# Optimization experiments

Measured on AMD Instinct MI355X. Metric: run time of the kernel, lower is better.

The kernel has to match this reference:

```python
import jax, jax.numpy as jnp
import numpy as np

NUM_NODES = 100000
N = 65536          # subgraph nodes returned by LastNeighborLoader
E = 655360         # N * size(=10) last-neighbor edges
B = 4096           # temporal event batch
MEM = 128          # memory_dim (== pos_embedding_dim)
TIME = 64          # time_dim
MSG = 64           # raw_msg_dim
EMB = 128          # embedding_dim (gnn out_channels)
HEADS = 2
HD = EMB // HEADS  # 64, TransformerConv out_channels//2 per head
HID = 64           # mlp_hidden_dim[-1]
IN = 2 * MEM       # gnn in_channels (memory || pos memory)
EDGE_D = MSG + TIME


def setup_inputs() -> dict:
    key = jax.random.key(0)
    ks = jax.random.split(key, 32)
    nrm = lambda i, shp, s=1.0: jax.random.normal(ks[i], shp, jnp.float32) * s
    inp = {}
    # data / state tensors
    inp["memory"] = nrm(0, (NUM_NODES, MEM))
    inp["pos_memory"] = nrm(1, (NUM_NODES, MEM))
    inp["last_update"] = jax.random.uniform(ks[2], (NUM_NODES,), jnp.float32) * 1000.0
    inp["n_id"] = jnp.arange(N, dtype=jnp.int32)
    inp["edge_index"] = jax.random.randint(ks[3], (2, E), 0, N, dtype=jnp.int32)
    inp["edge_t"] = jax.random.uniform(ks[4], (E,), jnp.float32) * 1000.0
    inp["edge_msg"] = nrm(5, (E, MSG))
    inp["src"] = jax.random.randint(ks[6], (B,), 0, N, dtype=jnp.int32)
    inp["dst"] = jax.random.randint(ks[7], (B,), 0, N, dtype=jnp.int32)
    inp["neg_dst"] = jax.random.randint(ks[8], (B,), 0, N, dtype=jnp.int32)
    # learned parameters
    inp["time_w"] = nrm(9, (1, TIME))                      # TimeEncoder Linear(1, time_dim)
    inp["time_b"] = nrm(10, (TIME,), 0.1)
    sI = 1.0 / np.sqrt(IN); sE = 1.0 / np.sqrt(EDGE_D)
    inp["Wq"] = nrm(11, (IN, HEADS * HD), sI); inp["bq"] = jnp.zeros((HEADS * HD,), jnp.float32)
    inp["Wk"] = nrm(12, (IN, HEADS * HD), sI); inp["bk"] = jnp.zeros((HEADS * HD,), jnp.float32)
    inp["Wv"] = nrm(13, (IN, HEADS * HD), sI); inp["bv"] = jnp.zeros((HEADS * HD,), jnp.float32)
    inp["We"] = nrm(14, (EDGE_D, HEADS * HD), sE); inp["be"] = jnp.zeros((HEADS * HD,), jnp.float32)
    inp["Wskip"] = nrm(15, (IN, EMB), sI); inp["bskip"] = jnp.zeros((EMB,), jnp.float32)
    inp["mlp_w"] = nrm(16, (EMB, HID), 1.0 / np.sqrt(EMB)); inp["mlp_b"] = jnp.zeros((HID,), jnp.float32)
    sH = 1.0 / np.sqrt(HID)
    inp["lps_w"] = nrm(17, (HID, HID), sH); inp["lps_b"] = jnp.zeros((HID,), jnp.float32)
    inp["lpd_w"] = nrm(18, (HID, HID), sH); inp["lpd_b"] = jnp.zeros((HID,), jnp.float32)
    inp["lpf_w"] = nrm(19, (HID, 1), sH); inp["lpf_b"] = jnp.zeros((1,), jnp.float32)
    return inp


def reference(memory, pos_memory, last_update, n_id, edge_index, edge_t, edge_msg,
              src, dst, neg_dst, time_w, time_b, Wq, bq, Wk, bk, Wv, bv, We, be,
              Wskip, bskip, mlp_w, mlp_b, lps_w, lps_b, lpd_w, lpd_b, lpf_w, lpf_b):
    Nn = n_id.shape[0]
    # assoc remap: global node id -> local row in subgraph
    assoc = jnp.zeros((NUM_NODES,), jnp.int32).at[n_id].set(jnp.arange(Nn, dtype=jnp.int32))
    # memory read + positional memory concat  -> [N, 2*MEM]
    z = jnp.concatenate([memory[n_id], pos_memory[n_id]], axis=-1)
    lu = last_update[n_id]                                # [N]
    se, de = edge_index[0], edge_index[1]                 # source (j), target (i)
    # time encoding of relative time: cos(Linear(1->TIME))
    rel_t = lu[se] - edge_t                               # [E]
    t_enc = jnp.cos(rel_t[:, None] * time_w[0][None, :] + time_b)  # [E, TIME]
    edge_attr = jnp.concatenate([t_enc, edge_msg], axis=-1)        # [E, TIME+MSG]
    # TransformerConv (heads=2, concat): q from target, k/v from source (+edge)
    q = (z @ Wq + bq).reshape(Nn, HEADS, HD)
    k = (z @ Wk + bk).reshape(Nn, HEADS, HD)
    v = (z @ Wv + bv).reshape(Nn, HEADS, HD)
    e = (edge_attr @ We + be).reshape(-1, HEADS, HD)
    ke = k[se] + e                                        # [E, H, HD]
    ve = v[se] + e
    score = jnp.sum(q[de] * ke, axis=-1) / jnp.sqrt(jnp.float32(HD))  # [E, H]
    # segment softmax over incoming edges of each target node
    smax = jax.ops.segment_max(score, de, num_segments=Nn)
    ex = jnp.exp(score - smax[de])
    denom = jax.ops.segment_sum(ex, de, num_segments=Nn)
    alpha = ex / (denom[de] + 1e-16)                      # [E, H]
    agg = jax.ops.segment_sum(alpha[..., None] * ve, de, num_segments=Nn)  # [N, H, HD]
    out = agg.reshape(Nn, HEADS * HD) + (z @ Wskip + bskip)  # root/skip connection
    # MLP([embedding_dim, hidden]) -> single Linear (last layer: no act/norm)
    h = out @ mlp_w + mlp_b                               # [N, HID]
    z_src = h[assoc[src]]; z_dst = h[assoc[dst]]; z_neg = h[assoc[neg_dst]]
    def link_pred(a, b):
        hh = jax.nn.relu(a @ lps_w + lps_b + b @ lpd_w + lpd_b)
        return hh @ lpf_w + lpf_b
    pos_out = link_pred(z_src, z_dst)                     # [B, 1]
    neg_out = link_pred(z_src, z_neg)                     # [B, 1]
    return pos_out, neg_out
```

## Files before the change

kernel.cpp:

```cpp
#include <hip/hip_runtime.h>
#include <math.h>

#define NNODES 100000
#define NSUB   65536
#define NEDGE  655360
#define NBATCH 4096
#define LDK 72

typedef __attribute__((ext_vector_type(8))) short short8;
typedef __attribute__((ext_vector_type(4))) float f32x4;

__device__ __forceinline__ unsigned short f2bf(float x) {
  unsigned int b = __float_as_uint(x);
  b += 0x7fffu + ((b >> 16) & 1u);
  return (unsigned short)(b >> 16);
}
__device__ __forceinline__ float bf2f(unsigned short u) {
  return __uint_as_float(((unsigned int)u) << 16);
}
__device__ __forceinline__ unsigned int pk2(float a, float b) {
  return (unsigned int)f2bf(a) | ((unsigned int)f2bf(b) << 16);
}

__global__ void k_sentinel(float* out) { out[0] = -12345.0f; }

__global__ void k_packW(const float* __restrict__ Wq, const float* __restrict__ bq,
                        const float* __restrict__ Wk, const float* __restrict__ bk,
                        const float* __restrict__ Wv, const float* __restrict__ bv,
                        const float* __restrict__ Ws, const float* __restrict__ bs,
                        const float* __restrict__ We,
                        unsigned short* __restrict__ Wt, float* __restrict__ bias) {
  int n = blockIdx.x, r = threadIdx.x;
  float v = 0.f, bn = 0.f;
  if (n < 128) { v = Wq[r * 128 + n]; bn = bq[n]; }
  else if (n < 256) { int i = n - 128, l = i >> 1, h = i & 1; v = Wk[r * 128 + h * 64 + l]; bn = bk[h * 64 + l]; }
  else if (n < 384) { int i = n - 256, l = i >> 1, h = i & 1; v = Wv[r * 128 + h * 64 + l]; bn = bv[h * 64 + l]; }
  else if (n < 512) { int c = n - 384; v = Ws[r * 128 + c]; bn = bs[c]; }
  else {
    int i = n - 512, h = i >> 7, kk = i & 127;
    float s = 0.f;
    for (int c = 0; c < 64; c++) s += Wq[r * 128 + h * 64 + c] * We[kk * 128 + h * 64 + c];
    v = s;
    if (r == 0) { float sb = 0.f; for (int c = 0; c < 64; c++) sb += bq[h * 64 + c] * We[kk * 128 + h * 64 + c]; bn = sb; }
  }
  Wt[(size_t)n * 256 + r] = f2bf(v);
  if (r == 0) bias[n] = bn;
}

__global__ void k_packW2(const float* __restrict__ We, const float* __restrict__ mlp_w,
                         unsigned short* __restrict__ W2t) {
  int r = blockIdx.x, j = threadIdx.x;
  float v;
  if (r < 128) v = mlp_w[r * 64 + j];
  else if (r < 192) { int k = r - 128; float s = 0; for (int c = 0; c < 64; c++) s += We[k * 128 + c] * mlp_w[c * 64 + j]; v = s; }
  else if (r < 256) { int k = r - 192; float s = 0; for (int c = 0; c < 64; c++) s += We[(64 + k) * 128 + c] * mlp_w[c * 64 + j]; v = s; }
  else if (r < 320) { int k = r - 256; float s = 0; for (int c = 0; c < 64; c++) s += We[k * 128 + 64 + c] * mlp_w[(64 + c) * 64 + j]; v = s; }
  else if (r < 384) { int k = r - 320; float s = 0; for (int c = 0; c < 64; c++) s += We[(64 + k) * 128 + 64 + c] * mlp_w[(64 + c) * 64 + j]; v = s; }
  else v = mlp_w[(r - 384) * 64 + j];
  W2t[(size_t)j * 512 + r] = f2bf(v);
}

__global__ void k_bem(const float* __restrict__ be, const float* __restrict__ mlp_w,
                      float* __restrict__ bem) {
  int h = blockIdx.x, j = threadIdx.x;
  float s = 0.f;
  for (int c = 0; c < 64; c++) s += be[h * 64 + c] * mlp_w[(h * 64 + c) * 64 + j];
  bem[h * 64 + j] = s;
}

__global__ void k_assoc(const int* __restrict__ n_id, int* __restrict__ assoc) {
  int i = blockIdx.x * 256 + threadIdx.x;
  if (i < NSUB) assoc[n_id[i]] = i;
}

__global__ void k_relt(const int* __restrict__ edge_index, const int* __restrict__ n_id,
                       const float* __restrict__ last_update, const float* __restrict__ edge_t,
                       float* __restrict__ rel_t) {
  int e = blockIdx.x * 256 + threadIdx.x;
  if (e < NEDGE) rel_t[e] = last_update[n_id[edge_index[e]]] - edge_t[e];
}

__global__ void k_deg(const int* __restrict__ edge_index, int* __restrict__ deg) {
  int e = blockIdx.x * 256 + threadIdx.x;
  if (e < NEDGE) atomicAdd(&deg[edge_index[NEDGE + e]], 1);
}

__global__ __launch_bounds__(1024)
void k_scan(const int* __restrict__ deg, int* __restrict__ offs, int* __restrict__ cursor) {
  __shared__ int wsum[16];
  __shared__ int carry_s;
  int t = threadIdx.x, w = t >> 6, l = t & 63;
  if (t == 0) carry_s = 0;
  __syncthreads();
  for (int base = 0; base < NSUB; base += 1024) {
    int i = base + t;
    int v = deg[i];
    int s = v;
    #pragma unroll
    for (int d = 1; d < 64; d <<= 1) {
      int u = __shfl_up(s, d, 64);
      if (l >= d) s += u;
    }
    if (l == 63) wsum[w] = s;
    __syncthreads();
    int woff = 0;
    for (int k2 = 0; k2 < w; k2++) woff += wsum[k2];
    int total = 0;
    for (int k2 = 0; k2 < 16; k2++) total += wsum[k2];
    int c = carry_s;
    int excl = c + woff + s - v;
    offs[i] = excl; cursor[i] = excl;
    __syncthreads();
    if (t == 0) carry_s = c + total;
    __syncthreads();
  }
  if (t == 0) { offs[NSUB] = carry_s; cursor[NSUB] = carry_s; }
}

__global__ void k_scatter(const int* __restrict__ edge_index, int* __restrict__ cursor,
                          int* __restrict__ csr) {
  int e = blockIdx.x * 256 + threadIdx.x;
  if (e < NEDGE) {
    int p = atomicAdd(&cursor[edge_index[NEDGE + e]], 1);
    csr[p] = e;
  }
}

__global__ __launch_bounds__(256)
void k_gemm_node(const float* __restrict__ mem, const float* __restrict__ pmem,
                 const int* __restrict__ n_id, const unsigned short* __restrict__ Wt,
                 const float* __restrict__ bias, unsigned short* __restrict__ nodeout) {
  __shared__ unsigned short sA[128][LDK];
  __shared__ unsigned short sB[128][LDK];
  int t = threadIdx.x;
  int row0 = blockIdx.x * 128, n0 = blockIdx.y * 128;
  int ar = t >> 1, ak = (t & 1) * 32;
  int nid = n_id[row0 + ar];
  const float* arow0 = mem + (size_t)nid * 128;
  const float* arow1 = pmem + (size_t)nid * 128;
  int br = t >> 1;
  int w = t >> 6, lane = t & 63, quad = lane >> 4, r16 = lane & 15;
  int m_off = (w >> 1) * 64, n_off = (w & 1) * 64;
  f32x4 acc[4][4] = {};
  for (int st = 0; st < 4; st++) {
    int ks = st * 64;
    const float* src = (ks < 128) ? (arow0 + ks + ak) : (arow1 + (ks - 128) + ak);
    __syncthreads();
    #pragma unroll
    for (int i = 0; i < 8; i++) {
      float4 f = *(const float4*)(src + i * 4);
      *(uint2*)&sA[ar][ak + i * 4] = make_uint2(pk2(f.x, f.y), pk2(f.z, f.w));
    }
    #pragma unroll
    for (int j = 0; j < 4; j++) {
      int c = (t & 1) * 4 + j;
      *(uint4*)&sB[br][c * 8] = *(const uint4*)(Wt + (size_t)(n0 + br) * 256 + ks + c * 8);
    }
    __syncthreads();
    #pragma unroll
    for (int kk = 0; kk < 2; kk++) {
      short8 af[4], bf_[4];
      #pragma unroll
      for (int i = 0; i < 4; i++) af[i]  = *(const short8*)&sA[m_off + i * 16 + r16][kk * 32 + quad * 8];
      #pragma unroll
      for (int i = 0; i < 4; i++) bf_[i] = *(const short8*)&sB[n_off + i * 16 + r16][kk * 32 + quad * 8];
      #pragma unroll
      for (int i = 0; i < 4; i++)
        #pragma unroll
        for (int j = 0; j < 4; j++)
          acc[i][j] = __builtin_amdgcn_mfma_f32_16x16x32_bf16(af[i], bf_[j], acc[i][j], 0, 0, 0);
    }
  }
  #pragma unroll
  for (int j = 0; j < 4; j++) {
    int col = n0 + n_off + j * 16 + r16;
    float bv_ = bias[col];
    #pragma unroll
    for (int i = 0; i < 4; i++) {
      int rbase = row0 + m_off + i * 16 + quad * 4;
      #pragma unroll
      for (int rg = 0; rg < 4; rg++)
        nodeout[(size_t)(rbase + rg) * 768 + col] = f2bf(acc[i][j][rg] + bv_);
    }
  }
}

__global__ __launch_bounds__(256)
void k_edge(const unsigned short* __restrict__ nodeout, const int* __restrict__ edge_index,
            const float* __restrict__ rel_t, const float* __restrict__ edge_msg,
            const float* __restrict__ time_w, const float* __restrict__ time_b,
            const float* __restrict__ be, const int* __restrict__ offs,
            const int* __restrict__ csr, unsigned short* __restrict__ aggbuf,
            float* __restrict__ salph) {
  int t = threadIdx.x, w = t >> 6, l = t & 63;
  int node = blockIdx.x * 4 + w;
  const unsigned short* nr = nodeout + (size_t)node * 768;
  float q0 = bf2f(nr[l]),       q1 = bf2f(nr[64 + l]);
  float qc0 = bf2f(nr[512 + l]), qm0 = bf2f(nr[576 + l]);
  float qc1 = bf2f(nr[640 + l]), qm1 = bf2f(nr[704 + l]);
  float tw = time_w[l], tb = time_b[l];
  float qbe0 = q0 * be[l], qbe1 = q1 * be[64 + l];
  #pragma unroll
  for (int s = 1; s < 64; s <<= 1) { qbe0 += __shfl_xor(qbe0, s, 64); qbe1 += __shfl_xor(qbe1, s, 64); }
  float m0 = -INFINITY, m1 = -INFINITY, d0 = 0.f, d1 = 0.f;
  float aV0 = 0, aV1 = 0, aC0 = 0, aM0 = 0, aC1 = 0, aM1 = 0;
  int e0 = offs[node], e1 = offs[node + 1];
  for (int idx = e0; idx < e1; idx++) {
    int eid = csr[idx];
    int se = edge_index[eid];
    float rt = rel_t[eid];
    const unsigned short* ns = nodeout + (size_t)se * 768;
    unsigned int kv = *(const unsigned int*)(ns + 128 + 2 * l);
    unsigned int vv = *(const unsigned int*)(ns + 256 + 2 * l);
    float mg = edge_msg[(size_t)eid * 64 + l];
    float cv = __cosf(rt * tw + tb);
    float k0 = bf2f((unsigned short)kv), k1 = bf2f((unsigned short)(kv >> 16));
    float v0 = bf2f((unsigned short)vv), v1 = bf2f((unsigned short)(vv >> 16));
    float p0 = q0 * k0 + qc0 * cv + qm0 * mg;
    float p1 = q1 * k1 + qc1 * cv + qm1 * mg;
    #pragma unroll
    for (int s = 1; s < 64; s <<= 1) { p0 += __shfl_xor(p0, s, 64); p1 += __shfl_xor(p1, s, 64); }
    float s0 = (p0 + qbe0) * 0.125f, s1 = (p1 + qbe1) * 0.125f;
    float nm0 = fmaxf(m0, s0), nm1 = fmaxf(m1, s1);
    float sc0 = __expf(m0 - nm0), sc1 = __expf(m1 - nm1);
    float w0 = __expf(s0 - nm0), w1 = __expf(s1 - nm1);
    d0 = d0 * sc0 + w0; d1 = d1 * sc1 + w1;
    aV0 = aV0 * sc0 + w0 * v0; aC0 = aC0 * sc0 + w0 * cv; aM0 = aM0 * sc0 + w0 * mg;
    aV1 = aV1 * sc1 + w1 * v1; aC1 = aC1 * sc1 + w1 * cv; aM1 = aM1 * sc1 + w1 * mg;
    m0 = nm0; m1 = nm1;
  }
  float i0 = 1.f / (d0 + 1e-16f), i1 = 1.f / (d1 + 1e-16f);
  unsigned short* ag = aggbuf + (size_t)node * 512;
  ag[l]       = f2bf(aV0 * i0); ag[64 + l]  = f2bf(aV1 * i1);
  ag[128 + l] = f2bf(aC0 * i0); ag[192 + l] = f2bf(aM0 * i0);
  ag[256 + l] = f2bf(aC1 * i1); ag[320 + l] = f2bf(aM1 * i1);
  ag[384 + l] = nr[384 + l];    ag[448 + l] = nr[448 + l];
  if (l == 0) { salph[node * 2] = d0 * i0; salph[node * 2 + 1] = d1 * i1; }
}

__global__ __launch_bounds__(128)
void k_gemm_final(const unsigned short* __restrict__ aggbuf, const unsigned short* __restrict__ W2t,
                  const float* __restrict__ salph, const float* __restrict__ bem,
                  const float* __restrict__ mlp_b, float* __restrict__ h) {
  __shared__ unsigned short sA[128][LDK];
  __shared__ unsigned short sB[64][LDK];
  int t = threadIdx.x;
  int row0 = blockIdx.x * 128;
  int w = t >> 6, lane = t & 63, quad = lane >> 4, r16 = lane & 15;
  int m_off = w * 64;
  f32x4 acc[4][4] = {};
  for (int st = 0; st < 8; st++) {
    int ks = st * 64;
    __syncthreads();
    #pragma unroll
    for (int c = 0; c < 8; c++)
      *(uint4*)&sA[t][c * 8] = *(const uint4*)(aggbuf + (size_t)(row0 + t) * 512 + ks + c * 8);
    int brr = t >> 1;
    #pragma unroll
    for (int j = 0; j < 4; j++) {
      int c = (t & 1) * 4 + j;
      *(uint4*)&sB[brr][c * 8] = *(const uint4*)(W2t + (size_t)brr * 512 + ks + c * 8);
    }
    __syncthreads();
    #pragma unroll
    for (int kk = 0; kk < 2; kk++) {
      short8 af[4], bf_[4];
      #pragma unroll
      for (int i = 0; i < 4; i++) af[i]  = *(const short8*)&sA[m_off + i * 16 + r16][kk * 32 + quad * 8];
      #pragma unroll
      for (int i = 0; i < 4; i++) bf_[i] = *(const short8*)&sB[i * 16 + r16][kk * 32 + quad * 8];
      #pragma unroll
      for (int i = 0; i < 4; i++)
        #pragma unroll
        for (int j = 0; j < 4; j++)
          acc[i][j] = __builtin_amdgcn_mfma_f32_16x16x32_bf16(af[i], bf_[j], acc[i][j], 0, 0, 0);
    }
  }
  #pragma unroll
  for (int j = 0; j < 4; j++) {
    int col = j * 16 + r16;
    float mb = mlp_b[col], b0 = bem[col], b1 = bem[64 + col];
    #pragma unroll
    for (int i = 0; i < 4; i++) {
      int rbase = row0 + m_off + i * 16 + quad * 4;
      #pragma unroll
      for (int rg = 0; rg < 4; rg++) {
        int rr = rbase + rg;
        h[(size_t)rr * 64 + col] = acc[i][j][rg] + mb + salph[rr * 2] * b0 + salph[rr * 2 + 1] * b1;
      }
    }
  }
}

__global__ __launch_bounds__(256)
void k_linkpred(const float* __restrict__ h, const int* __restrict__ assoc,
                const int* __restrict__ src, const int* __restrict__ dst,
                const int* __restrict__ neg, const float* __restrict__ lps_w,
                const float* __restrict__ lps_b, const float* __restrict__ lpd_w,
                const float* __restrict__ lpd_b, const float* __restrict__ lpf_w,
                const float* __restrict__ lpf_b, float* __restrict__ out) {
  int t = threadIdx.x, w = t >> 6, j = t & 63;
  int b = blockIdx.x * 4 + w;
  const float* hs = h + (size_t)assoc[src[b]] * 64;
  const float* hd = h + (size_t)assoc[dst[b]] * 64;
  const float* hn = h + (size_t)assoc[neg[b]] * 64;
  float vs = lps_b[j], vd = lpd_b[j], vn = lpd_b[j];
  for (int k = 0; k < 64; k++) {
    float ws_ = lps_w[k * 64 + j];
    float wd_ = lpd_w[k * 64 + j];
    vs += hs[k] * ws_;
    vd += hd[k] * wd_;
    vn += hn[k] * wd_;
  }
  float fw = lpf_w[j];
  float hp = fmaxf(vs + vd, 0.f) * fw;
  float hq = fmaxf(vs + vn, 0.f) * fw;
  #pragma unroll
  for (int m = 1; m < 64; m <<= 1) {
    hp += __shfl_xor(hp, m, 64);
    hq += __shfl_xor(hq, m, 64);
  }
  if (j == 0) {
    out[b] = hp + lpf_b[0];
    out[NBATCH + b] = hq + lpf_b[0];
  }
}

extern "C" void kernel_launch(void* const* d_in, const int* in_sizes, int n_in,
                              void* d_out, int out_size, void* d_ws, size_t ws_size,
                              hipStream_t stream) {
  if (n_in < 30) return;
  const float* memory      = (const float*)d_in[0];
  const float* pos_memory  = (const float*)d_in[1];
  const float* last_update = (const float*)d_in[2];
  const int*   n_id        = (const int*)d_in[3];
  const int*   edge_index  = (const int*)d_in[4];
  const float* edge_t      = (const float*)d_in[5];
  const float* edge_msg    = (const float*)d_in[6];
  const int*   src         = (const int*)d_in[7];
  const int*   dst         = (const int*)d_in[8];
  const int*   neg_dst     = (const int*)d_in[9];
  const float* time_w      = (const float*)d_in[10];
  const float* time_b      = (const float*)d_in[11];
  const float* Wq = (const float*)d_in[12]; const float* bq = (const float*)d_in[13];
  const float* Wk = (const float*)d_in[14]; const float* bk = (const float*)d_in[15];
  const float* Wv = (const float*)d_in[16]; const float* bv = (const float*)d_in[17];
  const float* We = (const float*)d_in[18]; const float* be = (const float*)d_in[19];
  const float* Wskip = (const float*)d_in[20]; const float* bskip = (const float*)d_in[21];
  const float* mlp_w = (const float*)d_in[22]; const float* mlp_b = (const float*)d_in[23];
  const float* lps_w = (const float*)d_in[24]; const float* lps_b = (const float*)d_in[25];
  const float* lpd_w = (const float*)d_in[26]; const float* lpd_b = (const float*)d_in[27];
  const float* lpf_w = (const float*)d_in[28]; const float* lpf_b = (const float*)d_in[29];
  float* out = (float*)d_out;

  char* ws = (char*)d_ws;
  size_t off = 0;
  auto alloc = [&](size_t bytes) -> void* {
    void* p = ws + off;
    off += (bytes + 255) & ~(size_t)255;
    return p;
  };
  int*   assoc   = (int*)alloc((size_t)NNODES * 4);
  unsigned short* Wt  = (unsigned short*)alloc((size_t)768 * 256 * 2);
  float* bias    = (float*)alloc(768 * 4);
  unsigned short* W2t = (unsigned short*)alloc((size_t)64 * 512 * 2);
  float* bem     = (float*)alloc(128 * 4);
  float* rel_t   = (float*)alloc((size_t)NEDGE * 4);
  unsigned short* nodeout = (unsigned short*)alloc((size_t)NSUB * 768 * 2);
  unsigned short* aggbuf  = (unsigned short*)alloc((size_t)NSUB * 512 * 2);
  float* salph   = (float*)alloc((size_t)NSUB * 2 * 4);
  int*   deg     = (int*)alloc((size_t)NSUB * 4);
  int*   offs    = (int*)alloc((size_t)(NSUB + 1) * 4);
  int*   cursor  = (int*)alloc((size_t)(NSUB + 1) * 4);
  int*   csr     = (int*)alloc((size_t)NEDGE * 4);
  float* hbuf    = (float*)alloc((size_t)NSUB * 64 * 4);

  if (ws_size < off) {
    k_sentinel<<<1, 1, 0, stream>>>(out);
    return;
  }

  (void)hipMemsetAsync(deg, 0, (size_t)NSUB * 4, stream);
  k_packW<<<768, 256, 0, stream>>>(Wq, bq, Wk, bk, Wv, bv, Wskip, bskip, We, Wt, bias);
  k_packW2<<<512, 64, 0, stream>>>(We, mlp_w, W2t);
  k_bem<<<2, 64, 0, stream>>>(be, mlp_w, bem);
  k_assoc<<<NSUB / 256, 256, 0, stream>>>(n_id, assoc);
  k_relt<<<NEDGE / 256, 256, 0, stream>>>(edge_index, n_id, last_update, edge_t, rel_t);
  k_deg<<<NEDGE / 256, 256, 0, stream>>>(edge_index, deg);
  k_scan<<<1, 1024, 0, stream>>>(deg, offs, cursor);
  k_scatter<<<NEDGE / 256, 256, 0, stream>>>(edge_index, cursor, csr);
  k_gemm_node<<<dim3(NSUB / 128, 6), 256, 0, stream>>>(memory, pos_memory, n_id, Wt, bias, nodeout);
  k_edge<<<NSUB / 4, 256, 0, stream>>>(nodeout, edge_index, rel_t, edge_msg, time_w, time_b,
                                       be, offs, csr, aggbuf, salph);
  k_gemm_final<<<NSUB / 128, 128, 0, stream>>>(aggbuf, W2t, salph, bem, mlp_b, hbuf);
  k_linkpred<<<NBATCH / 4, 256, 0, stream>>>(hbuf, assoc, src, dst, neg_dst,
                                             lps_w, lps_b, lpd_w, lpd_b, lpf_w, lpf_b, out);
}
```

Measured before the change: 785.1 us.

## Vectorize edge attention with 16 lanes per node, pre-pack node inputs to bf16

The edge kernel now handles four nodes per wavefront: 16 lanes per node, with 16-byte bf16 and float4 loads. To support this, Q/K/V/edge-projection columns are interleaved by head and the 1/sqrt(HD) scale is folded into the packed weights. The online-softmax max tracking is removed, so raw exponentials are summed, which saves per-edge work but could overflow for large scores. A separate kernel gathers and converts memory/pos_memory to bf16 once, instead of six times across the GEMM column blocks. The rel_t and degree kernels are fused into one launch.

```diff
diff --git a/kernel.cpp b/kernel.cpp
--- a/kernel.cpp
+++ b/kernel.cpp
@@ -18,8 +18,19 @@
 __device__ __forceinline__ float bf2f(unsigned short u) {
   return __uint_as_float(((unsigned int)u) << 16);
 }
+__device__ __forceinline__ float bflo(unsigned int u) { return __uint_as_float(u << 16); }
+__device__ __forceinline__ float bfhi(unsigned int u) { return __uint_as_float(u & 0xffff0000u); }
 __device__ __forceinline__ unsigned int pk2(float a, float b) {
   return (unsigned int)f2bf(a) | ((unsigned int)f2bf(b) << 16);
+}
+__device__ __forceinline__ void unpack8(uint4 u, float* a, float* b) {
+  a[0] = bflo(u.x); b[0] = bfhi(u.x);
+  a[1] = bflo(u.y); b[1] = bfhi(u.y);
+  a[2] = bflo(u.z); b[2] = bfhi(u.z);
+  a[3] = bflo(u.w); b[3] = bfhi(u.w);
+}
+__device__ __forceinline__ ushort4 pkv4(float a, float b, float c, float d) {
+  return make_ushort4(f2bf(a), f2bf(b), f2bf(c), f2bf(d));
 }
 
 __global__ void k_sentinel(float* out) { out[0] = -12345.0f; }
@@ -32,16 +43,29 @@
                         unsigned short* __restrict__ Wt, float* __restrict__ bias) {
   int n = blockIdx.x, r = threadIdx.x;
   float v = 0.f, bn = 0.f;
-  if (n < 128) { v = Wq[r * 128 + n]; bn = bq[n]; }
-  else if (n < 256) { int i = n - 128, l = i >> 1, h = i & 1; v = Wk[r * 128 + h * 64 + l]; bn = bk[h * 64 + l]; }
-  else if (n < 384) { int i = n - 256, l = i >> 1, h = i & 1; v = Wv[r * 128 + h * 64 + l]; bn = bv[h * 64 + l]; }
-  else if (n < 512) { int c = n - 384; v = Ws[r * 128 + c]; bn = bs[c]; }
-  else {
-    int i = n - 512, h = i >> 7, kk = i & 127;
+  if (n < 128) {
+    int l = n >> 1, h = n & 1;
+    v = Wq[r * 128 + h * 64 + l] * 0.125f; bn = bq[h * 64 + l] * 0.125f;
+  } else if (n < 256) {
+    int i = n - 128, l = i >> 1, h = i & 1;
+    v = Wk[r * 128 + h * 64 + l]; bn = bk[h * 64 + l];
+  } else if (n < 384) {
+    int i = n - 256, l = i >> 1, h = i & 1;
+    v = Wv[r * 128 + h * 64 + l]; bn = bv[h * 64 + l];
+  } else if (n < 512) {
+    int c = n - 384; v = Ws[r * 128 + c]; bn = bs[c];
+  } else {
+    int i = (n < 640) ? (n - 512) : (n - 640);
+    int c = i >> 1, h = i & 1;
+    int kk = (n < 640) ? c : (64 + c);
     float s = 0.f;
-    for (int c = 0; c < 64; c++) s += Wq[r * 128 + h * 64 + c] * We[kk * 128 + h * 64 + c];
-    v = s;
-    if (r == 0) { float sb = 0.f; for (int c = 0; c < 64; c++) sb += bq[h * 64 + c] * We[kk * 128 + h * 64 + c]; bn = sb; }
+    for (int d = 0; d < 64; d++) s += Wq[r * 128 + h * 64 + d] * We[kk * 128 + h * 64 + d];
+    v = s * 0.125f;
+    if (r == 0) {
+      float sb = 0.f;
+      for (int d = 0; d < 64; d++) sb += bq[h * 64 + d] * We[kk * 128 + h * 64 + d];
+      bn = sb * 0.125f;
+    }
   }
   Wt[(size_t)n * 256 + r] = f2bf(v);
   if (r == 0) bias[n] = bn;
@@ -73,16 +97,28 @@
   if (i < NSUB) assoc[n_id[i]] = i;
 }
 
-__global__ void k_relt(const int* __restrict__ edge_index, const int* __restrict__ n_id,
-                       const float* __restrict__ last_update, const float* __restrict__ edge_t,
-                       float* __restrict__ rel_t) {
+__global__ void k_packA(const float* __restrict__ mem, const float* __restrict__ pmem,
+                        const int* __restrict__ n_id, unsigned short* __restrict__ anodes) {
+  int i = blockIdx.x * 256 + threadIdx.x;
+  int node = i >> 5, ch = i & 31;
+  int nid = n_id[node];
+  const float* src = (ch < 16) ? (mem + (size_t)nid * 128 + ch * 8)
+                               : (pmem + (size_t)nid * 128 + (ch - 16) * 8);
+  float4 f0 = *(const float4*)src, f1 = *(const float4*)(src + 4);
+  uint4 o;
+  o.x = pk2(f0.x, f0.y); o.y = pk2(f0.z, f0.w);
+  o.z = pk2(f1.x, f1.y); o.w = pk2(f1.z, f1.w);
+  *(uint4*)(anodes + (size_t)node * 256 + ch * 8) = o;
+}
+
+__global__ void k_prep_edge(const int* __restrict__ edge_index, const int* __restrict__ n_id,
+                            const float* __restrict__ last_update, const float* __restrict__ edge_t,
+                            float* __restrict__ rel_t, int* __restrict__ deg) {
   int e = blockIdx.x * 256 + threadIdx.x;
-  if (e < NEDGE) rel_t[e] = last_update[n_id[edge_index[e]]] - edge_t[e];
-}
-
-__global__ void k_deg(const int* __restrict__ edge_index, int* __restrict__ deg) {
-  int e = blockIdx.x * 256 + threadIdx.x;
-  if (e < NEDGE) atomicAdd(&deg[edge_index[NEDGE + e]], 1);
+  if (e < NEDGE) {
+    rel_t[e] = last_update[n_id[edge_index[e]]] - edge_t[e];
+    atomicAdd(&deg[edge_index[NEDGE + e]], 1);
+  }
 }
 
 __global__ __launch_bounds__(1024)
@@ -127,35 +163,25 @@
 }
 
 __global__ __launch_bounds__(256)
-void k_gemm_node(const float* __restrict__ mem, const float* __restrict__ pmem,
-                 const int* __restrict__ n_id, const unsigned short* __restrict__ Wt,
+void k_gemm_node(const unsigned short* __restrict__ anodes, const unsigned short* __restrict__ Wt,
                  const float* __restrict__ bias, unsigned short* __restrict__ nodeout) {
   __shared__ unsigned short sA[128][LDK];
   __shared__ unsigned short sB[128][LDK];
   int t = threadIdx.x;
   int row0 = blockIdx.x * 128, n0 = blockIdx.y * 128;
   int ar = t >> 1, ak = (t & 1) * 32;
-  int nid = n_id[row0 + ar];
-  const float* arow0 = mem + (size_t)nid * 128;
-  const float* arow1 = pmem + (size_t)nid * 128;
-  int br = t >> 1;
   int w = t >> 6, lane = t & 63, quad = lane >> 4, r16 = lane & 15;
   int m_off = (w >> 1) * 64, n_off = (w & 1) * 64;
   f32x4 acc[4][4] = {};
   for (int st = 0; st < 4; st++) {
     int ks = st * 64;
-    const float* src = (ks < 128) ? (arow0 + ks + ak) : (arow1 + (ks - 128) + ak);
-    __syncthreads();
-    #pragma unroll
-    for (int i = 0; i < 8; i++) {
-      float4 f = *(const float4*)(src + i * 4);
-      *(uint2*)&sA[ar][ak + i * 4] = make_uint2(pk2(f.x, f.y), pk2(f.z, f.w));
-    }
-    #pragma unroll
-    for (int j = 0; j < 4; j++) {
-      int c = (t & 1) * 4 + j;
-      *(uint4*)&sB[br][c * 8] = *(const uint4*)(Wt + (size_t)(n0 + br) * 256 + ks + c * 8);
-    }
+    __syncthreads();
+    #pragma unroll
+    for (int i = 0; i < 4; i++)
+      *(uint4*)&sA[ar][ak + i * 8] = *(const uint4*)(anodes + (size_t)(row0 + ar) * 256 + ks + ak + i * 8);
+    #pragma unroll
+    for (int i = 0; i < 4; i++)
+      *(uint4*)&sB[ar][ak + i * 8] = *(const uint4*)(Wt + (size_t)(n0 + ar) * 256 + ks + ak + i * 8);
     __syncthreads();
     #pragma unroll
     for (int kk = 0; kk < 2; kk++) {
@@ -192,50 +218,68 @@
             const float* __restrict__ be, const int* __restrict__ offs,
             const int* __restrict__ csr, unsigned short* __restrict__ aggbuf,
             float* __restrict__ salph) {
-  int t = threadIdx.x, w = t >> 6, l = t & 63;
-  int node = blockIdx.x * 4 + w;
+  int t = threadIdx.x, w = t >> 6, lane = t & 63;
+  int j = lane & 15;
+  int node = blockIdx.x * 16 + w * 4 + (lane >> 4);
   const unsigned short* nr = nodeout + (size_t)node * 768;
-  float q0 = bf2f(nr[l]),       q1 = bf2f(nr[64 + l]);
-  float qc0 = bf2f(nr[512 + l]), qm0 = bf2f(nr[576 + l]);
-  float qc1 = bf2f(nr[640 + l]), qm1 = bf2f(nr[704 + l]);
-  float tw = time_w[l], tb = time_b[l];
-  float qbe0 = q0 * be[l], qbe1 = q1 * be[64 + l];
+  uint4 q4  = *(const uint4*)(nr + 8 * j);
+  uint4 qc4 = *(const uint4*)(nr + 512 + 8 * j);
+  uint4 qm4 = *(const uint4*)(nr + 640 + 8 * j);
+  float4 tw4 = *(const float4*)(time_w + 4 * j);
+  float4 tb4 = *(const float4*)(time_b + 4 * j);
+  float4 beA = *(const float4*)(be + 4 * j);
+  float4 beB = *(const float4*)(be + 64 + 4 * j);
+  float q0[4], q1[4], qc0[4], qc1[4], qm0[4], qm1[4];
+  unpack8(q4, q0, q1); unpack8(qc4, qc0, qc1); unpack8(qm4, qm0, qm1);
+  float qbe0 = q0[0] * beA.x + q0[1] * beA.y + q0[2] * beA.z + q0[3] * beA.w;
+  float qbe1 = q1[0] * beB.x + q1[1] * beB.y + q1[2] * beB.z + q1[3] * beB.w;
   #pragma unroll
-  for (int s = 1; s < 64; s <<= 1) { qbe0 += __shfl_xor(qbe0, s, 64); qbe1 += __shfl_xor(qbe1, s, 64); }
-  float m0 = -INFINITY, m1 = -INFINITY, d0 = 0.f, d1 = 0.f;
-  float aV0 = 0, aV1 = 0, aC0 = 0, aM0 = 0, aC1 = 0, aM1 = 0;
+  for (int s = 1; s < 16; s <<= 1) { qbe0 += __shfl_xor(qbe0, s, 64); qbe1 += __shfl_xor(qbe1, s, 64); }
+  float d0 = 0.f, d1 = 0.f;
+  float aV0[4] = {}, aV1[4] = {}, aC0[4] = {}, aC1[4] = {}, aM0[4] = {}, aM1[4] = {};
   int e0 = offs[node], e1 = offs[node + 1];
   for (int idx = e0; idx < e1; idx++) {
     int eid = csr[idx];
     int se = edge_index[eid];
     float rt = rel_t[eid];
     const unsigned short* ns = nodeout + (size_t)se * 768;
-    unsigned int kv = *(const unsigned int*)(ns + 128 + 2 * l);
-    unsigned int vv = *(const unsigned int*)(ns + 256 + 2 * l);
-    float mg = edge_msg[(size_t)eid * 64 + l];
-    float cv = __cosf(rt * tw + tb);
-    float k0 = bf2f((unsigned short)kv), k1 = bf2f((unsigned short)(kv >> 16));
-    float v0 = bf2f((unsigned short)vv), v1 = bf2f((unsigned short)(vv >> 16));
-    float p0 = q0 * k0 + qc0 * cv + qm0 * mg;
-    float p1 = q1 * k1 + qc1 * cv + qm1 * mg;
-    #pragma unroll
-    for (int s = 1; s < 64; s <<= 1) { p0 += __shfl_xor(p0, s, 64); p1 += __shfl_xor(p1, s, 64); }
-    float s0 = (p0 + qbe0) * 0.125f, s1 = (p1 + qbe1) * 0.125f;
-    float nm0 = fmaxf(m0, s0), nm1 = fmaxf(m1, s1);
-    float sc0 = __expf(m0 - nm0), sc1 = __expf(m1 - nm1);
-    float w0 = __expf(s0 - nm0), w1 = __expf(s1 - nm1);
-    d0 = d0 * sc0 + w0; d1 = d1 * sc1 + w1;
-    aV0 = aV0 * sc0 + w0 * v0; aC0 = aC0 * sc0 + w0 * cv; aM0 = aM0 * sc0 + w0 * mg;
-    aV1 = aV1 * sc1 + w1 * v1; aC1 = aC1 * sc1 + w1 * cv; aM1 = aM1 * sc1 + w1 * mg;
-    m0 = nm0; m1 = nm1;
+    uint4 kv = *(const uint4*)(ns + 128 + 8 * j);
+    uint4 vv = *(const uint4*)(ns + 256 + 8 * j);
+    float4 mg = *(const float4*)(edge_msg + (size_t)eid * 64 + 4 * j);
+    float k0[4], k1[4], v0[4], v1[4];
+    unpack8(kv, k0, k1); unpack8(vv, v0, v1);
+    float cv[4];
+    cv[0] = __cosf(rt * tw4.x + tb4.x);
+    cv[1] = __cosf(rt * tw4.y + tb4.y);
+    cv[2] = __cosf(rt * tw4.z + tb4.z);
+    cv[3] = __cosf(rt * tw4.w + tb4.w);
+    float p0 = q0[0] * k0[0] + q0[1] * k0[1] + q0[2] * k0[2] + q0[3] * k0[3]
+             + qc0[0] * cv[0] + qc0[1] * cv[1] + qc0[2] * cv[2] + qc0[3] * cv[3]
+             + qm0[0] * mg.x + qm0[1] * mg.y + qm0[2] * mg.z + qm0[3] * mg.w;
+    float p1 = q1[0] * k1[0] + q1[1] * k1[1] + q1[2] * k1[2] + q1[3] * k1[3]
+             + qc1[0] * cv[0] + qc1[1] * cv[1] + qc1[2] * cv[2] + qc1[3] * cv[3]
+             + qm1[0] * mg.x + qm1[1] * mg.y + qm1[2] * mg.z + qm1[3] * mg.w;
+    #pragma unroll
+    for (int s = 1; s < 16; s <<= 1) { p0 += __shfl_xor(p0, s, 64); p1 += __shfl_xor(p1, s, 64); }
+    float ex0 = __expf(p0 + qbe0), ex1 = __expf(p1 + qbe1);
+    d0 += ex0; d1 += ex1;
+    float mgc[4] = {mg.x, mg.y, mg.z, mg.w};
+    #pragma unroll
+    for (int c = 0; c < 4; c++) {
+      aV0[c] += ex0 * v0[c]; aC0[c] += ex0 * cv[c]; aM0[c] += ex0 * mgc[c];
+      aV1[c] += ex1 * v1[c]; aC1[c] += ex1 * cv[c]; aM1[c] += ex1 * mgc[c];
+    }
   }
   float i0 = 1.f / (d0 + 1e-16f), i1 = 1.f / (d1 + 1e-16f);
   unsigned short* ag = aggbuf + (size_t)node * 512;
-  ag[l]       = f2bf(aV0 * i0); ag[64 + l]  = f2bf(aV1 * i1);
-  ag[128 + l] = f2bf(aC0 * i0); ag[192 + l] = f2bf(aM0 * i0);
-  ag[256 + l] = f2bf(aC1 * i1); ag[320 + l] = f2bf(aM1 * i1);
-  ag[384 + l] = nr[384 + l];    ag[448 + l] = nr[448 + l];
-  if (l == 0) { salph[node * 2] = d0 * i0; salph[node * 2 + 1] = d1 * i1; }
+  *(ushort4*)(ag + 4 * j)       = pkv4(aV0[0] * i0, aV0[1] * i0, aV0[2] * i0, aV0[3] * i0);
+  *(ushort4*)(ag + 64 + 4 * j)  = pkv4(aV1[0] * i1, aV1[1] * i1, aV1[2] * i1, aV1[3] * i1);
+  *(ushort4*)(ag + 128 + 4 * j) = pkv4(aC0[0] * i0, aC0[1] * i0, aC0[2] * i0, aC0[3] * i0);
+  *(ushort4*)(ag + 192 + 4 * j) = pkv4(aM0[0] * i0, aM0[1] * i0, aM0[2] * i0, aM0[3] * i0);
+  *(ushort4*)(ag + 256 + 4 * j) = pkv4(aC1[0] * i1, aC1[1] * i1, aC1[2] * i1, aC1[3] * i1);
+  *(ushort4*)(ag + 320 + 4 * j) = pkv4(aM1[0] * i1, aM1[1] * i1, aM1[2] * i1, aM1[3] * i1);
+  *(uint4*)(ag + 384 + 8 * j)   = *(const uint4*)(nr + 384 + 8 * j);
+  if (j == 0) { salph[node * 2] = d0 * i0; salph[node * 2 + 1] = d1 * i1; }
 }
 
 __global__ __launch_bounds__(128)
@@ -257,8 +301,8 @@
       *(uint4*)&sA[t][c * 8] = *(const uint4*)(aggbuf + (size_t)(row0 + t) * 512 + ks + c * 8);
     int brr = t >> 1;
     #pragma unroll
-    for (int j = 0; j < 4; j++) {
-      int c = (t & 1) * 4 + j;
+    for (int jj = 0; jj < 4; jj++) {
+      int c = (t & 1) * 4 + jj;
       *(uint4*)&sB[brr][c * 8] = *(const uint4*)(W2t + (size_t)brr * 512 + ks + c * 8);
     }
     __syncthreads();
@@ -272,13 +316,13 @@
       #pragma unroll
       for (int i = 0; i < 4; i++)
         #pragma unroll
-        for (int j = 0; j < 4; j++)
-          acc[i][j] = __builtin_amdgcn_mfma_f32_16x16x32_bf16(af[i], bf_[j], acc[i][j], 0, 0, 0);
+        for (int jj = 0; jj < 4; jj++)
+          acc[i][jj] = __builtin_amdgcn_mfma_f32_16x16x32_bf16(af[i], bf_[jj], acc[i][jj], 0, 0, 0);
     }
   }
   #pragma unroll
-  for (int j = 0; j < 4; j++) {
-    int col = j * 16 + r16;
+  for (int jj = 0; jj < 4; jj++) {
+    int col = jj * 16 + r16;
     float mb = mlp_b[col], b0 = bem[col], b1 = bem[64 + col];
     #pragma unroll
     for (int i = 0; i < 4; i++) {
@@ -286,7 +330,7 @@
       #pragma unroll
       for (int rg = 0; rg < 4; rg++) {
         int rr = rbase + rg;
-        h[(size_t)rr * 64 + col] = acc[i][j][rg] + mb + salph[rr * 2] * b0 + salph[rr * 2 + 1] * b1;
+        h[(size_t)rr * 64 + col] = acc[i][jj][rg] + mb + salph[rr * 2] * b0 + salph[rr * 2 + 1] * b1;
       }
     }
   }
@@ -366,6 +410,7 @@
   unsigned short* W2t = (unsigned short*)alloc((size_t)64 * 512 * 2);
   float* bem     = (float*)alloc(128 * 4);
   float* rel_t   = (float*)alloc((size_t)NEDGE * 4);
+  unsigned short* anodes  = (unsigned short*)alloc((size_t)NSUB * 256 * 2);
   unsigned short* nodeout = (unsigned short*)alloc((size_t)NSUB * 768 * 2);
   unsigned short* aggbuf  = (unsigned short*)alloc((size_t)NSUB * 512 * 2);
   float* salph   = (float*)alloc((size_t)NSUB * 2 * 4);
@@ -385,13 +430,13 @@
   k_packW2<<<512, 64, 0, stream>>>(We, mlp_w, W2t);
   k_bem<<<2, 64, 0, stream>>>(be, mlp_w, bem);
   k_assoc<<<NSUB / 256, 256, 0, stream>>>(n_id, assoc);
-  k_relt<<<NEDGE / 256, 256, 0, stream>>>(edge_index, n_id, last_update, edge_t, rel_t);
-  k_deg<<<NEDGE / 256, 256, 0, stream>>>(edge_index, deg);
+  k_packA<<<NSUB * 32 / 256, 256, 0, stream>>>(memory, pos_memory, n_id, anodes);
+  k_prep_edge<<<NEDGE / 256, 256, 0, stream>>>(edge_index, n_id, last_update, edge_t, rel_t, deg);
   k_scan<<<1, 1024, 0, stream>>>(deg, offs, cursor);
   k_scatter<<<NEDGE / 256, 256, 0, stream>>>(edge_index, cursor, csr);
-  k_gemm_node<<<dim3(NSUB / 128, 6), 256, 0, stream>>>(memory, pos_memory, n_id, Wt, bias, nodeout);
-  k_edge<<<NSUB / 4, 256, 0, stream>>>(nodeout, edge_index, rel_t, edge_msg, time_w, time_b,
-                                       be, offs, csr, aggbuf, salph);
+  k_gemm_node<<<dim3(NSUB / 128, 6), 256, 0, stream>>>(anodes, Wt, bias, nodeout);
+  k_edge<<<NSUB / 16, 256, 0, stream>>>(nodeout, edge_index, rel_t, edge_msg, time_w, time_b,
+                                        be, offs, csr, aggbuf, salph);
   k_gemm_final<<<NSUB / 128, 128, 0, stream>>>(aggbuf, W2t, salph, bem, mlp_b, hbuf);
   k_linkpred<<<NBATCH / 4, 256, 0, stream>>>(hbuf, assoc, src, dst, neg_dst,
                                              lps_w, lps_b, lpd_w, lpd_b, lpf_w, lpf_b, out);
```

Result: faster. 741.6 us (-5.5%).
